# Performance work log

Hardware: AMD Instinct MI355X
Metric: run time of the kernel (lower is better)

Reference implementation:

```python
import jax, jax.numpy as jnp
import numpy as np

# ---- static configuration (mirrors init_kwargs) ----
B, NCAM = 1, 6
FC, FH, FW = 128, 16, 44              # featureShape
ORFH, ORFW = 128, 352                 # transformedImgShape H, W
D_ST, D_END, D_STEP = 1.0, 49.0, 1.0
D = int(np.arange(D_ST, D_END, D_STEP).shape[0])   # 48 depth bins
OUTC = 128
XB = (-50.0, 50.0, 1.0)
YB = (-50.0, 50.0, 1.0)
BEV_H = int((YB[1] - YB[0]) / YB[2])  # 100
BEV_W = int((XB[1] - XB[0]) / XB[2])  # 100
THRESH = 0.05                         # opacity_filter
ERR_TOL = 1.0                         # error_tolerance
COV_DILATE = 0.3                      # 3DGS low-pass on 2D cov diagonal
ALPHA_MAX = 0.99
ALPHA_MIN = 1.0 / 255.0
BN_EPS = 1e-3


def _frustum():
    ds = jnp.arange(D_ST, D_END, D_STEP, dtype=jnp.float32)[:, None, None]
    xs = jnp.linspace(0.0, ORFW - 1.0, FW, dtype=jnp.float32)[None, None, :]
    ys = jnp.linspace(0.0, ORFH - 1.0, FH, dtype=jnp.float32)[None, :, None]
    shp = (D, FH, FW)
    return jnp.stack([jnp.broadcast_to(xs, shp), jnp.broadcast_to(ys, shp),
                      jnp.broadcast_to(ds, shp)], axis=-1)  # [D,FH,FW,3]


def _conv(x, w, b, pad):
    y = jax.lax.conv_general_dilated(x, w, (1, 1), [(pad, pad), (pad, pad)],
                                     dimension_numbers=('NCHW', 'OIHW', 'NCHW'))
    return y + b[None, :, None, None]


def _bn(x, g, beta, m, v):
    # eval-mode BatchNorm2d with running stats
    inv = g / jnp.sqrt(v + BN_EPS)
    return (x - m[None, :, None, None]) * inv[None, :, None, None] + beta[None, :, None, None]


def _rasterize(features, means, cov6, opac):
    """Differentiable BEV Gaussian splatting (alpha compositing in index order).
    features [G,C], means [G,3] (normalized to [-1,1]), cov6 [G,6]=(xx,xy,xz,yy,yz,zz), opac [G].
    """
    h, w = BEV_H, BEV_W
    sh, sw = h / 2.0, w / 2.0                 # h/FoVy, w/FoVx with FoV=2
    op = jnp.where(opac > THRESH, opac, 0.0)  # opacity cull (variable-length mask in torch)
    # full_proj_transform: row0 -> row index (y), row1 -> col index (x)
    py = h / 2.0 - sh * means[:, 1]
    px = w / 2.0 - sw * means[:, 0]
    # 2D covariance in (py,px) basis: J Sigma3 J^T with J = [[0,-sh,0],[-sw,0,0]]
    a = sh * sh * cov6[:, 3] + COV_DILATE     # var along py (from Sigma_yy)
    b = sh * sw * cov6[:, 1]                  # cov(py,px) (from Sigma_xy)
    c = sw * sw * cov6[:, 0] + COV_DILATE     # var along px (from Sigma_xx)
    det = a * c - b * b
    op = jnp.where(det > 0.0, op, 0.0)
    inv_det = 1.0 / jnp.where(det > 0.0, det, 1.0)
    ys = jnp.arange(h, dtype=jnp.float32)
    xs = jnp.arange(w, dtype=jnp.float32)
    dy = py[None, :] - ys[:, None]            # [h,G]
    dx = px[None, :] - xs[:, None]            # [w,G]
    # power = -0.5 d^T Sigma2^{-1} d, Sigma2^{-1} = [[c,-b],[-b,a]]/det
    power = (-0.5 * (c * inv_det) * dy * dy)[:, None, :] \
            + (-0.5 * (a * inv_det) * dx * dx)[None, :, :] \
            + (b * inv_det) * dy[:, None, :] * dx[None, :, :]   # [h,w,G]
    alpha = jnp.minimum(ALPHA_MAX, op * jnp.exp(jnp.minimum(power, 0.0)))
    alpha = jnp.where(alpha < ALPHA_MIN, 0.0, alpha)
    T = jnp.cumprod(1.0 - alpha, axis=-1)
    T_excl = jnp.concatenate([jnp.ones_like(T[..., :1]), T[..., :-1]], axis=-1)
    wgt = alpha * T_excl                      # [h,w,G]
    bev = jnp.einsum('hwg,gc->chw', wgt, features)   # bg color = 0
    return bev


def reference(cam2ego_rot, cam2ego_trans, cam_intrins, post_cam2ego_rot, post_cam2ego_trans,
              img_feats, conv1_w, conv1_b, bn1_g, bn1_b, bn1_m, bn1_v,
              conv2_w, conv2_b, bn2_g, bn2_b, bn2_m, bn2_v, conv3_w, conv3_b):
    # --- geometry lifting ---
    frustum = _frustum()                                             # [D,FH,FW,3]
    pts = frustum[None, None] - post_cam2ego_trans[:, :, None, None, None, :]
    pts = jnp.einsum('bnij,bndhwj->bndhwi', jnp.linalg.inv(post_cam2ego_rot), pts)
    pts = jnp.concatenate([pts[..., :2] * pts[..., 2:3], pts[..., 2:3]], axis=-1)
    combine = cam2ego_rot @ jnp.linalg.inv(cam_intrins)
    geometry = jnp.einsum('bnij,bndhwj->bndhwi', combine, pts) \
               + cam2ego_trans[:, :, None, None, None, :]            # [B,N,D,FH,FW,3]
    # --- depth net ---
    x = img_feats.reshape(B * NCAM, FC, FH, FW)
    x = jax.nn.relu(_bn(_conv(x, conv1_w, conv1_b, 1), bn1_g, bn1_b, bn1_m, bn1_v))
    x = jax.nn.relu(_bn(_conv(x, conv2_w, conv2_b, 1), bn2_g, bn2_b, bn2_m, bn2_v))
    x = _conv(x, conv3_w, conv3_b, 0)                                # [B*N, OUTC+D+1, H, W]
    depth_prob = jax.nn.softmax(x[:, :D], axis=1).reshape(B, NCAM, D, FH, FW)
    opac = jax.nn.sigmoid(x[:, D:D + 1]).reshape(B, NCAM, FH, FW)
    feats = x[:, D + 1:].reshape(B, NCAM, OUTC, FH, FW)
    # --- per-pixel Gaussian moments over the depth distribution ---
    means3d = jnp.einsum('bndhw,bndhwi->bnhwi', depth_prob, geometry)
    delta = means3d[:, :, None] - geometry                           # [B,N,D,FH,FW,3]
    cov = jnp.einsum('bndhw,bndhwi,bndhwj->bnhwij', depth_prob, delta, delta)
    cov = cov * (ERR_TOL ** 2 / 9.0)
    # --- normalize to BEV frame ---
    center = jnp.array([(XB[0] + XB[1]) / 2.0, (YB[0] + YB[1]) / 2.0, 0.0], jnp.float32)
    scale = jnp.array([2.0 / (XB[1] - XB[0]), 2.0 / (YB[1] - YB[0]), 1.0], jnp.float32)
    means_n = (means3d - center) * scale
    cov_n = cov * (scale[:, None] * scale[None, :])
    cov6 = jnp.stack([cov_n[..., 0, 0], cov_n[..., 0, 1], cov_n[..., 0, 2],
                      cov_n[..., 1, 1], cov_n[..., 1, 2], cov_n[..., 2, 2]], axis=-1)
    G = NCAM * FH * FW
    f = jnp.transpose(feats, (0, 1, 3, 4, 2)).reshape(B, G, OUTC)
    m = means_n.reshape(B, G, 3)
    c6 = cov6.reshape(B, G, 6)
    o = opac.reshape(B, G)
    bev = jax.vmap(_rasterize)(f, m, c6, o)                          # [B,OUTC,BEV_H,BEV_W]
    return bev


def setup_inputs() -> dict:
    key = jax.random.key(0)
    ks = jax.random.split(key, 16)
    eye = jnp.eye(3, dtype=jnp.float32)
    cam2ego_rot = eye + 0.05 * jax.random.normal(ks[0], (B, NCAM, 3, 3), jnp.float32)
    cam2ego_trans = 0.5 * jax.random.normal(ks[1], (B, NCAM, 3), jnp.float32)
    intr = jnp.array([[260.0, 0.0, ORFW / 2.0], [0.0, 260.0, ORFH / 2.0], [0.0, 0.0, 1.0]], jnp.float32)
    cam_intrins = jnp.broadcast_to(intr, (B, NCAM, 3, 3)) * (1.0 + 0.01 * jax.random.normal(ks[2], (B, NCAM, 1, 1), jnp.float32))
    post_cam2ego_rot = eye + 0.01 * jax.random.normal(ks[3], (B, NCAM, 3, 3), jnp.float32)
    post_cam2ego_trans = 2.0 * jax.random.normal(ks[4], (B, NCAM, 3), jnp.float32)
    img_feats = jax.random.normal(ks[5], (B, NCAM, FC, FH, FW), jnp.float32)
    def cw(k, o, i, kh, kw):
        return jax.random.normal(k, (o, i, kh, kw), jnp.float32) / np.sqrt(i * kh * kw)
    inp = dict(cam2ego_rot=cam2ego_rot, cam2ego_trans=cam2ego_trans, cam_intrins=cam_intrins,
               post_cam2ego_rot=post_cam2ego_rot, post_cam2ego_trans=post_cam2ego_trans,
               img_feats=img_feats,
               conv1_w=cw(ks[6], FC, FC, 3, 3), conv1_b=jnp.zeros((FC,), jnp.float32),
               bn1_g=jnp.ones((FC,), jnp.float32), bn1_b=0.1 * jax.random.normal(ks[7], (FC,), jnp.float32),
               bn1_m=jnp.zeros((FC,), jnp.float32), bn1_v=jnp.ones((FC,), jnp.float32),
               conv2_w=cw(ks[8], FC, FC, 3, 3), conv2_b=jnp.zeros((FC,), jnp.float32),
               bn2_g=jnp.ones((FC,), jnp.float32), bn2_b=0.1 * jax.random.normal(ks[9], (FC,), jnp.float32),
               bn2_m=jnp.zeros((FC,), jnp.float32), bn2_v=jnp.ones((FC,), jnp.float32),
               conv3_w=cw(ks[10], OUTC + D + 1, FC, 1, 1),
               conv3_b=jnp.zeros((OUTC + D + 1,), jnp.float32))
    return inp
```

## Files before the change

### kernel.cpp

```cpp
#include <hip/hip_runtime.h>
#include <math.h>

#define NCAM 6
#define FHh 16
#define FWw 44
#define PIX 704
#define FCc 128
#define DB 48
#define C3 177
#define C3PAD 192
#define KCONV 1152
#define NG 4224
#define BEVN 10000
#define NSPLIT 3
#define SG 1408
#define TH_LOG (-5.5412635f)

#define OFF_WT1    0
#define OFF_WT2    147456
#define OFF_WT3    294912
#define OFF_GEO    319488
#define OFF_X1     724992
#define OFF_X2     1265664
#define OFF_X3     1806336
#define OFF_PART   2553984
#define OFF_PRM    4716672
#define OFF_PRM2   4733568
#define OFF_FEATT  4742016
#define OFF_SF     0
#define OFF_SP     3840000

typedef __attribute__((ext_vector_type(8))) short bf16x8;
typedef __attribute__((ext_vector_type(4))) float f32x4;
typedef __attribute__((ext_vector_type(4))) int i32x4;

__device__ __forceinline__ unsigned short f2bf(float x) {
  unsigned u = __float_as_uint(x);
  return (unsigned short)((u + 0x7FFF + ((u >> 16) & 1)) >> 16);
}
__device__ __forceinline__ float bf2f(unsigned short h) {
  return __uint_as_float(((unsigned)h) << 16);
}

__device__ __forceinline__ void inv3(const float* A, float* I) {
  float a=A[0],b=A[1],c=A[2],d=A[3],e=A[4],f=A[5],g=A[6],h=A[7],i=A[8];
  float c0 = e*i - f*h, c1 = f*g - d*i, c2 = d*h - e*g;
  float det = a*c0 + b*c1 + c*c2;
  float id = 1.f/det;
  I[0]=c0*id; I[1]=(c*h-b*i)*id; I[2]=(b*f-c*e)*id;
  I[3]=c1*id; I[4]=(a*i-c*g)*id; I[5]=(c*d-a*f)*id;
  I[6]=c2*id; I[7]=(b*g-a*h)*id; I[8]=(a*e-b*d)*id;
}

__global__ void k_geom(const float* __restrict__ rot, const float* __restrict__ intr,
                       const float* __restrict__ post_rot,
                       const float* __restrict__ trans, const float* __restrict__ post_trans,
                       float* __restrict__ ws) {
  __shared__ float sm[NCAM][24];
  if (threadIdx.x < NCAM) {
    int n = threadIdx.x;
    float ip[9], ii[9];
    inv3(post_rot + n*9, ip);
    inv3(intr + n*9, ii);
    const float* R = rot + n*9;
    for (int j = 0; j < 9; ++j) sm[n][j] = ip[j];
    for (int r = 0; r < 3; ++r)
      for (int c = 0; c < 3; ++c) {
        float s = 0.f;
        for (int k = 0; k < 3; ++k) s += R[r*3+k]*ii[k*3+c];
        sm[n][9 + r*3 + c] = s;
      }
  }
  __syncthreads();
  int idx = blockIdx.x*256 + threadIdx.x;
  if (idx >= NCAM*DB*PIX) return;
  int n = idx / (DB*PIX);
  int rem = idx % (DB*PIX);
  int d = rem / PIX;
  int hw = rem % PIX;
  int h = hw / FWw, w = hw % FWw;
  float fx = w * (351.0f/43.0f);
  float fy = h * (127.0f/15.0f);
  float fz = 1.0f + (float)d;
  const float* pt = post_trans + n*3;
  float v0 = fx - pt[0], v1 = fy - pt[1], v2 = fz - pt[2];
  const float* m = sm[n];
  float x = m[0]*v0 + m[1]*v1 + m[2]*v2;
  float y = m[3]*v0 + m[4]*v1 + m[5]*v2;
  float z = m[6]*v0 + m[7]*v1 + m[8]*v2;
  float q0 = x*z, q1 = y*z, q2 = z;
  const float* c = m + 9;
  const float* t = trans + n*3;
  float gx = c[0]*q0 + c[1]*q1 + c[2]*q2 + t[0];
  float gy = c[3]*q0 + c[4]*q1 + c[5]*q2 + t[1];
  ((float2*)(ws + OFF_GEO))[idx] = make_float2(gx, gy);
}

__global__ void k_wtrans(const float* __restrict__ w1, const float* __restrict__ w2,
                         const float* __restrict__ w3, float* __restrict__ ws) {
  int e = blockIdx.x*256 + threadIdx.x;
  if (e < 147456) {
    float v1 = w1[e], v2 = w2[e];
    unsigned short h1 = f2bf(v1), h2 = f2bf(v2);
    unsigned short l1 = f2bf(v1 - bf2f(h1)), l2 = f2bf(v2 - bf2f(h2));
    unsigned short* wt1 = (unsigned short*)(ws + OFF_WT1);
    unsigned short* wt2 = (unsigned short*)(ws + OFF_WT2);
    wt1[e] = h1; wt1[147456 + e] = l1;
    wt2[e] = h2; wt2[147456 + e] = l2;
  }
  if (e < 192*128) {
    int oc = e >> 7, k = e & 127;
    float v = (oc < C3) ? w3[oc*FCc + k] : 0.f;
    unsigned short h = f2bf(v);
    unsigned short* wt3 = (unsigned short*)(ws + OFF_WT3);
    wt3[e] = h; wt3[24576 + e] = f2bf(v - bf2f(h));
  }
}

#define LROW 20

__global__ __launch_bounds__(256) void k_gemm_mfma(
    const float* __restrict__ in, const float* ws, float* __restrict__ part, int woff)
{
  __shared__ int alds[2][64*LROW];
  __shared__ int blds[2][64*LROW];
  int tid = threadIdx.x;
  int px0 = blockIdx.x * 64;
  int oc0 = blockIdx.y * 64;
  int z = blockIdx.z; int n = z >> 2, ks = z & 3;
  const unsigned short* whi = (const unsigned short*)(ws + woff);
  const unsigned short* wlo = whi + 147456;
  const float* inn = in + (size_t)n*FCc*PIX;
  int wv = tid >> 6, lane = tid & 63;
  int a_oc = tid >> 2, a_kq = tid & 3;
  int b_px = tid & 63, b_kq = tid >> 6;
  int p = px0 + b_px; int b_y = p / FWw, b_x = p - b_y*FWw;
  int k00 = ks * 288;

  i32x4 pa_h, pa_l; float bv[8];
  auto issueA = [&](int s) {
    size_t gi = (size_t)(oc0 + a_oc)*KCONV + (k00 + s*32 + a_kq*8);
    pa_h = *(const i32x4*)(whi + gi);
    pa_l = *(const i32x4*)(wlo + gi);
  };
  auto issueB = [&](int s) {
    #pragma unroll
    for (int j = 0; j < 8; ++j) {
      int k = k00 + s*32 + b_kq*8 + j;
      int ic = k / 9, tap = k - ic*9;
      int ky = tap / 3, kx = tap - ky*3;
      int yy = b_y + ky - 1, xx = b_x + kx - 1;
      float v = 0.f;
      if ((unsigned)yy < FHh && (unsigned)xx < FWw) v = inn[(size_t)ic*PIX + yy*FWw + xx];
      bv[j] = v;
    }
  };

  f32x4 a00 = {0.f,0.f,0.f,0.f}, a01 = a00, a10 = a00, a11 = a00;
  int ocr = (wv >> 1) * 32, pxr = (wv & 1) * 32;
  int dq = (lane >> 4) * 4;
  int rA0 = (ocr + (lane & 15)) * LROW + dq;
  int rA1 = rA0 + 16*LROW;
  int rB0 = (pxr + (lane & 15)) * LROW + dq;
  int rB1 = rB0 + 16*LROW;
  int aw = a_oc*LROW + a_kq*4;
  int bw = b_px*LROW + b_kq*4;

  issueA(0); issueB(0);
  for (int s = 0; s < 9; ++s) {
    __syncthreads();
    *(i32x4*)&alds[0][aw] = pa_h;
    *(i32x4*)&alds[1][aw] = pa_l;
    {
      i32x4 vh, vl;
      int th[8], tl[8];
      #pragma unroll
      for (int j = 0; j < 8; ++j) {
        unsigned short h = f2bf(bv[j]);
        th[j] = h; tl[j] = f2bf(bv[j] - bf2f(h));
      }
      vh.x = th[0]|(th[1]<<16); vh.y = th[2]|(th[3]<<16);
      vh.z = th[4]|(th[5]<<16); vh.w = th[6]|(th[7]<<16);
      vl.x = tl[0]|(tl[1]<<16); vl.y = tl[2]|(tl[3]<<16);
      vl.z = tl[4]|(tl[5]<<16); vl.w = tl[6]|(tl[7]<<16);
      *(i32x4*)&blds[0][bw] = vh;
      *(i32x4*)&blds[1][bw] = vl;
    }
    __syncthreads();
    if (s < 8) { issueA(s+1); issueB(s+1); }
    bf16x8 ah0 = *(bf16x8*)&alds[0][rA0], ah1 = *(bf16x8*)&alds[0][rA1];
    bf16x8 al0 = *(bf16x8*)&alds[1][rA0], al1 = *(bf16x8*)&alds[1][rA1];
    bf16x8 bh0 = *(bf16x8*)&blds[0][rB0], bh1 = *(bf16x8*)&blds[0][rB1];
    bf16x8 bl0 = *(bf16x8*)&blds[1][rB0], bl1 = *(bf16x8*)&blds[1][rB1];
    a00 = __builtin_amdgcn_mfma_f32_16x16x32_bf16(ah0, bh0, a00, 0, 0, 0);
    a01 = __builtin_amdgcn_mfma_f32_16x16x32_bf16(ah0, bh1, a01, 0, 0, 0);
    a10 = __builtin_amdgcn_mfma_f32_16x16x32_bf16(ah1, bh0, a10, 0, 0, 0);
    a11 = __builtin_amdgcn_mfma_f32_16x16x32_bf16(ah1, bh1, a11, 0, 0, 0);
    a00 = __builtin_amdgcn_mfma_f32_16x16x32_bf16(ah0, bl0, a00, 0, 0, 0);
    a01 = __builtin_amdgcn_mfma_f32_16x16x32_bf16(ah0, bl1, a01, 0, 0, 0);
    a10 = __builtin_amdgcn_mfma_f32_16x16x32_bf16(ah1, bl0, a10, 0, 0, 0);
    a11 = __builtin_amdgcn_mfma_f32_16x16x32_bf16(ah1, bl1, a11, 0, 0, 0);
    a00 = __builtin_amdgcn_mfma_f32_16x16x32_bf16(al0, bh0, a00, 0, 0, 0);
    a01 = __builtin_amdgcn_mfma_f32_16x16x32_bf16(al0, bh1, a01, 0, 0, 0);
    a10 = __builtin_amdgcn_mfma_f32_16x16x32_bf16(al1, bh0, a10, 0, 0, 0);
    a11 = __builtin_amdgcn_mfma_f32_16x16x32_bf16(al1, bh1, a11, 0, 0, 0);
  }
  float* pp = part + (size_t)(ks*NCAM + n)*FCc*PIX;
  int ocb = oc0 + ocr + ((lane >> 4) << 2);
  int pxb = px0 + pxr + (lane & 15);
  #pragma unroll
  for (int i = 0; i < 4; ++i) {
    pp[(size_t)(ocb + i)*PIX + pxb]           = a00[i];
    pp[(size_t)(ocb + i)*PIX + pxb + 16]      = a01[i];
    pp[(size_t)(ocb + 16 + i)*PIX + pxb]      = a10[i];
    pp[(size_t)(ocb + 16 + i)*PIX + pxb + 16] = a11[i];
  }
}

__global__ __launch_bounds__(256) void k_gemm_mfma3(
    const float* __restrict__ in, const float* ws,
    const float* __restrict__ bias, float* __restrict__ outbuf)
{
  __shared__ int alds[2][64*LROW];
  __shared__ int blds[2][64*LROW];
  int tid = threadIdx.x;
  int px0 = blockIdx.x * 64;
  int oc0 = blockIdx.y * 64;
  int n = blockIdx.z;
  const unsigned short* whi = (const unsigned short*)(ws + OFF_WT3);
  const unsigned short* wlo = whi + 24576;
  const float* inn = in + (size_t)n*FCc*PIX;
  int wv = tid >> 6, lane = tid & 63;
  int a_oc = tid >> 2, a_kq = tid & 3;
  int b_px = tid & 63, b_kq = tid >> 6;
  int p = px0 + b_px;

  i32x4 pa_h, pa_l; float bvv[8];
  auto issueA = [&](int s) {
    size_t gi = (size_t)(oc0 + a_oc)*128 + (s*32 + a_kq*8);
    pa_h = *(const i32x4*)(whi + gi);
    pa_l = *(const i32x4*)(wlo + gi);
  };
  auto issueB = [&](int s) {
    #pragma unroll
    for (int j = 0; j < 8; ++j) {
      int ic = s*32 + b_kq*8 + j;
      bvv[j] = inn[(size_t)ic*PIX + p];
    }
  };

  f32x4 a00 = {0.f,0.f,0.f,0.f}, a01 = a00, a10 = a00, a11 = a00;
  int ocr = (wv >> 1) * 32, pxr = (wv & 1) * 32;
  int dq = (lane >> 4) * 4;
  int rA0 = (ocr + (lane & 15)) * LROW + dq;
  int rA1 = rA0 + 16*LROW;
  int rB0 = (pxr + (lane & 15)) * LROW + dq;
  int rB1 = rB0 + 16*LROW;
  int aw = a_oc*LROW + a_kq*4;
  int bw = b_px*LROW + b_kq*4;

  issueA(0); issueB(0);
  for (int s = 0; s < 4; ++s) {
    __syncthreads();
    *(i32x4*)&alds[0][aw] = pa_h;
    *(i32x4*)&alds[1][aw] = pa_l;
    {
      i32x4 vh, vl;
      int th[8], tl[8];
      #pragma unroll
      for (int j = 0; j < 8; ++j) {
        unsigned short h = f2bf(bvv[j]);
        th[j] = h; tl[j] = f2bf(bvv[j] - bf2f(h));
      }
      vh.x = th[0]|(th[1]<<16); vh.y = th[2]|(th[3]<<16);
      vh.z = th[4]|(th[5]<<16); vh.w = th[6]|(th[7]<<16);
      vl.x = tl[0]|(tl[1]<<16); vl.y = tl[2]|(tl[3]<<16);
      vl.z = tl[4]|(tl[5]<<16); vl.w = tl[6]|(tl[7]<<16);
      *(i32x4*)&blds[0][bw] = vh;
      *(i32x4*)&blds[1][bw] = vl;
    }
    __syncthreads();
    if (s < 3) { issueA(s+1); issueB(s+1); }
    bf16x8 ah0 = *(bf16x8*)&alds[0][rA0], ah1 = *(bf16x8*)&alds[0][rA1];
    bf16x8 al0 = *(bf16x8*)&alds[1][rA0], al1 = *(bf16x8*)&alds[1][rA1];
    bf16x8 bh0 = *(bf16x8*)&blds[0][rB0], bh1 = *(bf16x8*)&blds[0][rB1];
    bf16x8 bl0 = *(bf16x8*)&blds[1][rB0], bl1 = *(bf16x8*)&blds[1][rB1];
    a00 = __builtin_amdgcn_mfma_f32_16x16x32_bf16(ah0, bh0, a00, 0, 0, 0);
    a01 = __builtin_amdgcn_mfma_f32_16x16x32_bf16(ah0, bh1, a01, 0, 0, 0);
    a10 = __builtin_amdgcn_mfma_f32_16x16x32_bf16(ah1, bh0, a10, 0, 0, 0);
    a11 = __builtin_amdgcn_mfma_f32_16x16x32_bf16(ah1, bh1, a11, 0, 0, 0);
    a00 = __builtin_amdgcn_mfma_f32_16x16x32_bf16(ah0, bl0, a00, 0, 0, 0);
    a01 = __builtin_amdgcn_mfma_f32_16x16x32_bf16(ah0, bl1, a01, 0, 0, 0);
    a10 = __builtin_amdgcn_mfma_f32_16x16x32_bf16(ah1, bl0, a10, 0, 0, 0);
    a11 = __builtin_amdgcn_mfma_f32_16x16x32_bf16(ah1, bl1, a11, 0, 0, 0);
    a00 = __builtin_amdgcn_mfma_f32_16x16x32_bf16(al0, bh0, a00, 0, 0, 0);
    a01 = __builtin_amdgcn_mfma_f32_16x16x32_bf16(al0, bh1, a01, 0, 0, 0);
    a10 = __builtin_amdgcn_mfma_f32_16x16x32_bf16(al1, bh0, a10, 0, 0, 0);
    a11 = __builtin_amdgcn_mfma_f32_16x16x32_bf16(al1, bh1, a11, 0, 0, 0);
  }
  int ocb = oc0 + ocr + ((lane >> 4) << 2);
  int pxb = px0 + pxr + (lane & 15);
  #pragma unroll
  for (int i = 0; i < 4; ++i) {
    int o0 = ocb + i, o1 = ocb + 16 + i;
    if (o0 < C3) {
      float b = bias[o0];
      outbuf[(size_t)(n*C3 + o0)*PIX + pxb]      = a00[i] + b;
      outbuf[(size_t)(n*C3 + o0)*PIX + pxb + 16] = a01[i] + b;
    }
    if (o1 < C3) {
      float b = bias[o1];
      outbuf[(size_t)(n*C3 + o1)*PIX + pxb]      = a10[i] + b;
      outbuf[(size_t)(n*C3 + o1)*PIX + pxb + 16] = a11[i] + b;
    }
  }
}

__global__ void k_epi_bn(const float* __restrict__ part, const float* __restrict__ cb,
                         const float* __restrict__ g, const float* __restrict__ be,
                         const float* __restrict__ mn, const float* __restrict__ vr,
                         float* __restrict__ out, int KSPLIT)
{
  int idx = blockIdx.x*256 + threadIdx.x;
  if (idx >= NCAM*FCc*176) return;
  int px4 = idx % 176;
  int t = idx / 176;
  int oc = t % FCc;
  int n = t / FCc;
  float4 s = {0.f,0.f,0.f,0.f};
  for (int ks = 0; ks < KSPLIT; ++ks) {
    const float4* p = (const float4*)(part + (size_t)((ks*NCAM+n)*FCc + oc)*PIX);
    float4 v = p[px4];
    s.x += v.x; s.y += v.y; s.z += v.z; s.w += v.w;
  }
  float inv = g[oc] * rsqrtf(vr[oc] + 1e-3f);
  float sh = (cb[oc] - mn[oc]) * inv + be[oc];
  float4 o;
  o.x = fmaxf(s.x*inv + sh, 0.f);
  o.y = fmaxf(s.y*inv + sh, 0.f);
  o.z = fmaxf(s.z*inv + sh, 0.f);
  o.w = fmaxf(s.w*inv + sh, 0.f);
  ((float4*)(out + (size_t)(n*FCc + oc)*PIX))[px4] = o;
}

__global__ void k_moments(float* __restrict__ ws) {
  int wid  = (blockIdx.x * 256 + threadIdx.x) >> 6;
  int lane = threadIdx.x & 63;
  int n = wid / PIX, hw = wid % PIX;
  const float* x3 = ws + OFF_X3 + (size_t)n*C3*PIX + hw;
  float logit = (lane < DB) ? x3[(size_t)lane*PIX] : -1e30f;
  float mx = logit;
  for (int off = 1; off < 64; off <<= 1) mx = fmaxf(mx, __shfl_xor(mx, off));
  float e = (lane < DB) ? expf(logit - mx) : 0.f;
  float s = e;
  for (int off = 1; off < 64; off <<= 1) s += __shfl_xor(s, off);
  float p = e / s;
  float gx = 0.f, gy = 0.f;
  if (lane < DB) {
    float2 g2 = ((const float2*)(ws + OFF_GEO))[(size_t)(n*DB + lane)*PIX + hw];
    gx = g2.x; gy = g2.y;
  }
  float sx = p*gx;
  for (int off = 1; off < 64; off <<= 1) sx += __shfl_xor(sx, off);
  float sy = p*gy;
  for (int off = 1; off < 64; off <<= 1) sy += __shfl_xor(sy, off);
  float dx = gx - sx, dy = gy - sy;
  float c00 = p*dx*dx, c01 = p*dx*dy, c11 = p*dy*dy;
  for (int off = 1; off < 64; off <<= 1) c00 += __shfl_xor(c00, off);
  for (int off = 1; off < 64; off <<= 1) c01 += __shfl_xor(c01, off);
  for (int off = 1; off < 64; off <<= 1) c11 += __shfl_xor(c11, off);
  float opl = x3[(size_t)DB*PIX];
  float opac = 1.f / (1.f + expf(-opl));
  float a = c11*(1.f/9.f) + 0.3f;
  float b = c01*(1.f/9.f);
  float c = c00*(1.f/9.f) + 0.3f;
  float py = 50.f - sy;
  float px = 50.f - sx;
  float det = a*c - b*b;
  float op = (opac > 0.05f) ? opac : 0.f;
  float invd = 1.f;
  if (det > 0.f) invd = 1.f/det; else op = 0.f;
  if (lane == 0) {
    float lop = (op > 0.f) ? logf(op) : -1e30f;
    ((float4*)(ws + OFF_PRM))[wid]  = make_float4(py, px, -0.5f*c*invd, -0.5f*a*invd);
    ((float2*)(ws + OFF_PRM2))[wid] = make_float2(b*invd, lop);
  }
  float* ft = ws + OFF_FEATT + (size_t)wid*128;
  ft[lane]      = x3[(size_t)(DB + 1 + lane)*PIX];
  ft[lane + 64] = x3[(size_t)(DB + 1 + lane + 64)*PIX];
}

template<int CTRL, int RMASK>
__device__ __forceinline__ float dpp_mul(float v) {
  int t = __builtin_amdgcn_update_dpp(0x3f800000, __float_as_int(v), CTRL, RMASK, 0xF, false);
  return v * __int_as_float(t);
}

__global__ __launch_bounds__(512) void k_raster(const float* __restrict__ ws,
                                                float* __restrict__ wsout) {
  __shared__ float4 s4[SG];
  __shared__ float2 s2[SG];
  int lane = threadIdx.x & 63, wv = threadIdx.x >> 6;
  int split = blockIdx.x / 1250;
  int pxb   = blockIdx.x % 1250;
  int pix = pxb * 8 + wv;
  float yi = (float)(pix / 100), xi = (float)(pix % 100);
  int gbase = split * SG;
  const float4* prm4 = (const float4*)(ws + OFF_PRM) + gbase;
  const float2* prm2 = (const float2*)(ws + OFF_PRM2) + gbase;
  const float2* ft = (const float2*)(ws + OFF_FEATT);
  for (int i = threadIdx.x; i < SG; i += 512) {
    s4[i] = prm4[i];
    s2[i] = prm2[i];
  }
  __syncthreads();
  float T = 1.f, ax = 0.f, ay = 0.f;
  for (int gl = 0; gl < SG; gl += 64) {
    float4 c4 = s4[gl + lane];
    float2 c2 = s2[gl + lane];
    float dyv = c4.x - yi, dxv = c4.y - xi;
    float pw = c4.z*dyv*dyv + c4.w*dxv*dxv + c2.x*dyv*dxv;
    float t  = pw + c2.y;
    bool hit = (t >= TH_LOG);
    unsigned long long m0 = __ballot(hit);
    if (m0) {
      float alpha = __expf(fminf(t, c2.y));
      alpha = fminf(alpha, 0.99f);
      alpha = hit ? alpha : 0.f;
      float P = 1.f - alpha;
      P = dpp_mul<0x111, 0xF>(P);
      P = dpp_mul<0x112, 0xF>(P);
      P = dpp_mul<0x114, 0xF>(P);
      P = dpp_mul<0x118, 0xF>(P);
      P = dpp_mul<0x142, 0xA>(P);
      P = dpp_mul<0x143, 0xC>(P);
      float E = __int_as_float(__builtin_amdgcn_update_dpp(
                  0x3f800000, __float_as_int(P), 0x138, 0xF, 0xF, false));
      float w = alpha * T * E;
      T *= __int_as_float(__builtin_amdgcn_readlane(__float_as_int(P), 63));
      unsigned long long mask = __ballot(w > 1e-9f);
      int g0 = gbase + gl;
      while (mask) {
        int jj[8];
        #pragma unroll
        for (int b = 0; b < 8; ++b) {
          if (mask) { jj[b] = __builtin_ctzll(mask); mask &= mask - 1ull; }
          else jj[b] = -1;
        }
        float2 fb[8]; float wb[8];
        #pragma unroll
        for (int b = 0; b < 8; ++b) {
          int j = (jj[b] >= 0) ? jj[b] : jj[0];
          fb[b] = ft[(size_t)(g0 + j)*64 + lane];
          wb[b] = (jj[b] >= 0)
            ? __int_as_float(__builtin_amdgcn_readlane(__float_as_int(w), jj[b]))
            : 0.f;
        }
        #pragma unroll
        for (int b = 0; b < 8; ++b) { ax += wb[b]*fb[b].x; ay += wb[b]*fb[b].y; }
      }
      if (T < 1e-7f) break;
    }
  }
  float* sf = wsout + OFF_SF + ((size_t)split*BEVN + pix)*128;
  sf[2*lane]   = ax;
  sf[2*lane+1] = ay;
  if (lane == 0) (wsout + OFF_SP)[split*BEVN + pix] = T;
}

__global__ __launch_bounds__(512) void k_combine(const float* __restrict__ ws,
                                                 float* __restrict__ out) {
  int lane = threadIdx.x & 63, wv = threadIdx.x >> 6;
  int pix = blockIdx.x * 8 + wv;
  const float* sp = ws + OFF_SP;
  float P0 = sp[pix], P1 = sp[BEVN + pix];
  const float2* f0 = (const float2*)(ws + OFF_SF + (size_t)pix*128);
  const float2* f1 = (const float2*)(ws + OFF_SF + ((size_t)BEVN + pix)*128);
  const float2* f2 = (const float2*)(ws + OFF_SF + ((size_t)2*BEVN + pix)*128);
  float2 a = f0[lane], b = f1[lane], c = f2[lane];
  float w1 = P0, w2 = P0*P1;
  float ox = a.x + w1*b.x + w2*c.x;
  float oy = a.y + w1*b.y + w2*c.y;
  out[(size_t)(2*lane)*BEVN + pix]   = ox;
  out[(size_t)(2*lane+1)*BEVN + pix] = oy;
}

extern "C" void kernel_launch(void* const* d_in, const int* in_sizes, int n_in,
                              void* d_out, int out_size, void* d_ws, size_t ws_size,
                              hipStream_t stream) {
  const float* rot        = (const float*)d_in[0];
  const float* trans      = (const float*)d_in[1];
  const float* intr       = (const float*)d_in[2];
  const float* post_rot   = (const float*)d_in[3];
  const float* post_trans = (const float*)d_in[4];
  const float* img        = (const float*)d_in[5];
  const float* w1  = (const float*)d_in[6];
  const float* b1  = (const float*)d_in[7];
  const float* g1  = (const float*)d_in[8];
  const float* be1 = (const float*)d_in[9];
  const float* m1  = (const float*)d_in[10];
  const float* v1  = (const float*)d_in[11];
  const float* w2  = (const float*)d_in[12];
  const float* b2  = (const float*)d_in[13];
  const float* g2  = (const float*)d_in[14];
  const float* be2 = (const float*)d_in[15];
  const float* m2  = (const float*)d_in[16];
  const float* v2  = (const float*)d_in[17];
  const float* w3  = (const float*)d_in[18];
  const float* b3  = (const float*)d_in[19];
  float* ws  = (float*)d_ws;
  float* out = (float*)d_out;

  k_wtrans<<<576, 256, 0, stream>>>(w1, w2, w3, ws);
  k_geom<<<792, 256, 0, stream>>>(rot, intr, post_rot, trans, post_trans, ws);

  k_gemm_mfma<<<dim3(11,2,24), 256, 0, stream>>>(img, ws, ws+OFF_PART, OFF_WT1);
  k_epi_bn<<<528, 256, 0, stream>>>(ws+OFF_PART, b1, g1, be1, m1, v1, ws+OFF_X1, 4);
  k_gemm_mfma<<<dim3(11,2,24), 256, 0, stream>>>(ws+OFF_X1, ws, ws+OFF_PART, OFF_WT2);
  k_epi_bn<<<528, 256, 0, stream>>>(ws+OFF_PART, b2, g2, be2, m2, v2, ws+OFF_X2, 4);
  k_gemm_mfma3<<<dim3(11,3,6), 256, 0, stream>>>(ws+OFF_X2, ws, b3, ws+OFF_X3);

  k_moments<<<1056, 256, 0, stream>>>(ws);
  k_raster<<<3750, 512, 0, stream>>>(ws, ws);
  k_combine<<<1250, 512, 0, stream>>>(ws, out);
}
```

Before: 123.4 us.

## Merge prep kernels, store splat features as bf16, use 1024-thread raster blocks

Merges the geometry and weight-conversion kernels into a single launch that branches on block index, removing one kernel launch. Splat features are now stored as packed bf16 pairs instead of fp32, halving the bytes the rasterizer gathers per contributing Gaussian. The raster kernel moves to 1024-thread blocks covering 16 pixels each, so every block's shared-memory parameter load serves twice as many pixels. The bf16 features lose precision against the fp32 reference, and the larger blocks may reduce scheduling flexibility when some waves exit early.

```diff
diff --git a/kernel.cpp b/kernel.cpp
--- a/kernel.cpp
+++ b/kernel.cpp
@@ -52,68 +52,68 @@
   I[6]=c2*id; I[7]=(b*g-a*h)*id; I[8]=(a*e-b*d)*id;
 }
 
-__global__ void k_geom(const float* __restrict__ rot, const float* __restrict__ intr,
+__global__ void k_prep(const float* __restrict__ rot, const float* __restrict__ intr,
                        const float* __restrict__ post_rot,
                        const float* __restrict__ trans, const float* __restrict__ post_trans,
-                       float* __restrict__ ws) {
-  __shared__ float sm[NCAM][24];
-  if (threadIdx.x < NCAM) {
-    int n = threadIdx.x;
-    float ip[9], ii[9];
-    inv3(post_rot + n*9, ip);
-    inv3(intr + n*9, ii);
-    const float* R = rot + n*9;
-    for (int j = 0; j < 9; ++j) sm[n][j] = ip[j];
-    for (int r = 0; r < 3; ++r)
-      for (int c = 0; c < 3; ++c) {
-        float s = 0.f;
-        for (int k = 0; k < 3; ++k) s += R[r*3+k]*ii[k*3+c];
-        sm[n][9 + r*3 + c] = s;
-      }
-  }
-  __syncthreads();
-  int idx = blockIdx.x*256 + threadIdx.x;
-  if (idx >= NCAM*DB*PIX) return;
-  int n = idx / (DB*PIX);
-  int rem = idx % (DB*PIX);
-  int d = rem / PIX;
-  int hw = rem % PIX;
-  int h = hw / FWw, w = hw % FWw;
-  float fx = w * (351.0f/43.0f);
-  float fy = h * (127.0f/15.0f);
-  float fz = 1.0f + (float)d;
-  const float* pt = post_trans + n*3;
-  float v0 = fx - pt[0], v1 = fy - pt[1], v2 = fz - pt[2];
-  const float* m = sm[n];
-  float x = m[0]*v0 + m[1]*v1 + m[2]*v2;
-  float y = m[3]*v0 + m[4]*v1 + m[5]*v2;
-  float z = m[6]*v0 + m[7]*v1 + m[8]*v2;
-  float q0 = x*z, q1 = y*z, q2 = z;
-  const float* c = m + 9;
-  const float* t = trans + n*3;
-  float gx = c[0]*q0 + c[1]*q1 + c[2]*q2 + t[0];
-  float gy = c[3]*q0 + c[4]*q1 + c[5]*q2 + t[1];
-  ((float2*)(ws + OFF_GEO))[idx] = make_float2(gx, gy);
-}
-
-__global__ void k_wtrans(const float* __restrict__ w1, const float* __restrict__ w2,
-                         const float* __restrict__ w3, float* __restrict__ ws) {
-  int e = blockIdx.x*256 + threadIdx.x;
-  if (e < 147456) {
-    float v1 = w1[e], v2 = w2[e];
-    unsigned short h1 = f2bf(v1), h2 = f2bf(v2);
-    unsigned short l1 = f2bf(v1 - bf2f(h1)), l2 = f2bf(v2 - bf2f(h2));
-    unsigned short* wt1 = (unsigned short*)(ws + OFF_WT1);
-    unsigned short* wt2 = (unsigned short*)(ws + OFF_WT2);
-    wt1[e] = h1; wt1[147456 + e] = l1;
-    wt2[e] = h2; wt2[147456 + e] = l2;
-  }
-  if (e < 192*128) {
-    int oc = e >> 7, k = e & 127;
-    float v = (oc < C3) ? w3[oc*FCc + k] : 0.f;
-    unsigned short h = f2bf(v);
-    unsigned short* wt3 = (unsigned short*)(ws + OFF_WT3);
-    wt3[e] = h; wt3[24576 + e] = f2bf(v - bf2f(h));
+                       const float* __restrict__ w1, const float* __restrict__ w2,
+                       const float* __restrict__ w3, float* __restrict__ ws) {
+  if (blockIdx.x < 792) {
+    __shared__ float sm[NCAM][24];
+    if (threadIdx.x < NCAM) {
+      int n = threadIdx.x;
+      float ip[9], ii[9];
+      inv3(post_rot + n*9, ip);
+      inv3(intr + n*9, ii);
+      const float* R = rot + n*9;
+      for (int j = 0; j < 9; ++j) sm[n][j] = ip[j];
+      for (int r = 0; r < 3; ++r)
+        for (int c = 0; c < 3; ++c) {
+          float s = 0.f;
+          for (int k = 0; k < 3; ++k) s += R[r*3+k]*ii[k*3+c];
+          sm[n][9 + r*3 + c] = s;
+        }
+    }
+    __syncthreads();
+    int idx = blockIdx.x*256 + threadIdx.x;
+    if (idx >= NCAM*DB*PIX) return;
+    int n = idx / (DB*PIX);
+    int rem = idx % (DB*PIX);
+    int d = rem / PIX;
+    int hw = rem % PIX;
+    int h = hw / FWw, w = hw % FWw;
+    float fx = w * (351.0f/43.0f);
+    float fy = h * (127.0f/15.0f);
+    float fz = 1.0f + (float)d;
+    const float* pt = post_trans + n*3;
+    float v0 = fx - pt[0], v1 = fy - pt[1], v2 = fz - pt[2];
+    const float* m = sm[n];
+    float x = m[0]*v0 + m[1]*v1 + m[2]*v2;
+    float y = m[3]*v0 + m[4]*v1 + m[5]*v2;
+    float z = m[6]*v0 + m[7]*v1 + m[8]*v2;
+    float q0 = x*z, q1 = y*z, q2 = z;
+    const float* c = m + 9;
+    const float* t = trans + n*3;
+    float gx = c[0]*q0 + c[1]*q1 + c[2]*q2 + t[0];
+    float gy = c[3]*q0 + c[4]*q1 + c[5]*q2 + t[1];
+    ((float2*)(ws + OFF_GEO))[idx] = make_float2(gx, gy);
+  } else {
+    int e = (blockIdx.x - 792)*256 + threadIdx.x;
+    if (e < 147456) {
+      float v1 = w1[e], v2 = w2[e];
+      unsigned short h1 = f2bf(v1), h2 = f2bf(v2);
+      unsigned short l1 = f2bf(v1 - bf2f(h1)), l2 = f2bf(v2 - bf2f(h2));
+      unsigned short* wt1 = (unsigned short*)(ws + OFF_WT1);
+      unsigned short* wt2 = (unsigned short*)(ws + OFF_WT2);
+      wt1[e] = h1; wt1[147456 + e] = l1;
+      wt2[e] = h2; wt2[147456 + e] = l2;
+    }
+    if (e < 192*128) {
+      int oc = e >> 7, k = e & 127;
+      float v = (oc < C3) ? w3[oc*FCc + k] : 0.f;
+      unsigned short h = f2bf(v);
+      unsigned short* wt3 = (unsigned short*)(ws + OFF_WT3);
+      wt3[e] = h; wt3[24576 + e] = f2bf(v - bf2f(h));
+    }
   }
 }
 
@@ -385,9 +385,9 @@
     ((float4*)(ws + OFF_PRM))[wid]  = make_float4(py, px, -0.5f*c*invd, -0.5f*a*invd);
     ((float2*)(ws + OFF_PRM2))[wid] = make_float2(b*invd, lop);
   }
-  float* ft = ws + OFF_FEATT + (size_t)wid*128;
-  ft[lane]      = x3[(size_t)(DB + 1 + lane)*PIX];
-  ft[lane + 64] = x3[(size_t)(DB + 1 + lane + 64)*PIX];
+  unsigned lo = f2bf(x3[(size_t)(DB + 1 + 2*lane)*PIX]);
+  unsigned hi = f2bf(x3[(size_t)(DB + 1 + 2*lane + 1)*PIX]);
+  ((unsigned*)(ws + OFF_FEATT))[(size_t)wid*64 + lane] = lo | (hi << 16);
 }
 
 template<int CTRL, int RMASK>
@@ -396,20 +396,20 @@
   return v * __int_as_float(t);
 }
 
-__global__ __launch_bounds__(512) void k_raster(const float* __restrict__ ws,
-                                                float* __restrict__ wsout) {
+__global__ __launch_bounds__(1024) void k_raster(const float* __restrict__ ws,
+                                                 float* __restrict__ wsout) {
   __shared__ float4 s4[SG];
   __shared__ float2 s2[SG];
   int lane = threadIdx.x & 63, wv = threadIdx.x >> 6;
-  int split = blockIdx.x / 1250;
-  int pxb   = blockIdx.x % 1250;
-  int pix = pxb * 8 + wv;
+  int split = blockIdx.x / 625;
+  int pxb   = blockIdx.x % 625;
+  int pix = pxb * 16 + wv;
   float yi = (float)(pix / 100), xi = (float)(pix % 100);
   int gbase = split * SG;
   const float4* prm4 = (const float4*)(ws + OFF_PRM) + gbase;
   const float2* prm2 = (const float2*)(ws + OFF_PRM2) + gbase;
-  const float2* ft = (const float2*)(ws + OFF_FEATT);
-  for (int i = threadIdx.x; i < SG; i += 512) {
+  const unsigned* ftu = (const unsigned*)(ws + OFF_FEATT);
+  for (int i = threadIdx.x; i < SG; i += 1024) {
     s4[i] = prm4[i];
     s2[i] = prm2[i];
   }
@@ -447,17 +447,20 @@
           if (mask) { jj[b] = __builtin_ctzll(mask); mask &= mask - 1ull; }
           else jj[b] = -1;
         }
-        float2 fb[8]; float wb[8];
+        unsigned ub[8]; float wb[8];
         #pragma unroll
         for (int b = 0; b < 8; ++b) {
           int j = (jj[b] >= 0) ? jj[b] : jj[0];
-          fb[b] = ft[(size_t)(g0 + j)*64 + lane];
+          ub[b] = ftu[(size_t)(g0 + j)*64 + lane];
           wb[b] = (jj[b] >= 0)
             ? __int_as_float(__builtin_amdgcn_readlane(__float_as_int(w), jj[b]))
             : 0.f;
         }
         #pragma unroll
-        for (int b = 0; b < 8; ++b) { ax += wb[b]*fb[b].x; ay += wb[b]*fb[b].y; }
+        for (int b = 0; b < 8; ++b) {
+          ax += wb[b]*bf2f((unsigned short)(ub[b] & 0xffff));
+          ay += wb[b]*bf2f((unsigned short)(ub[b] >> 16));
+        }
       }
       if (T < 1e-7f) break;
     }
@@ -511,8 +514,8 @@
   float* ws  = (float*)d_ws;
   float* out = (float*)d_out;
 
-  k_wtrans<<<576, 256, 0, stream>>>(w1, w2, w3, ws);
-  k_geom<<<792, 256, 0, stream>>>(rot, intr, post_rot, trans, post_trans, ws);
+  k_prep<<<1368, 256, 0, stream>>>(rot, intr, post_rot, trans, post_trans,
+                                   w1, w2, w3, ws);
 
   k_gemm_mfma<<<dim3(11,2,24), 256, 0, stream>>>(img, ws, ws+OFF_PART, OFF_WT1);
   k_epi_bn<<<528, 256, 0, stream>>>(ws+OFF_PART, b1, g1, be1, m1, v1, ws+OFF_X1, 4);
@@ -521,6 +524,6 @@
   k_gemm_mfma3<<<dim3(11,3,6), 256, 0, stream>>>(ws+OFF_X2, ws, b3, ws+OFF_X3);
 
   k_moments<<<1056, 256, 0, stream>>>(ws);
-  k_raster<<<3750, 512, 0, stream>>>(ws, ws);
+  k_raster<<<1875, 1024, 0, stream>>>(ws, ws);
   k_combine<<<1250, 512, 0, stream>>>(ws, out);
 }
```

After: 124.6 us. No clear change (+1.0%).
